# Kernel optimization log

Hardware: AMD Instinct MI355X
Metric: run time of the kernel (lower is better)

The kernel has to match this reference:

```python
import jax, jax.numpy as jnp
import numpy as np

EPS = 1e-5  # torch BatchNorm default

def _conv(x, w, pad):
    return jax.lax.conv_general_dilated(x, w, window_strides=(1, 1), padding=pad,
                                        dimension_numbers=('NCHW', 'OIHW', 'NCHW'))

def _bn(x, g, b, m, v):
    # eval-mode BatchNorm2d over channel axis 1 of NCHW
    scale = g / jnp.sqrt(v + EPS)
    return x * scale[None, :, None, None] + (b - m * scale)[None, :, None, None]

def _bn1d(x, g, b, m, v):
    scale = g / jnp.sqrt(v + EPS)
    return x * scale[None, :] + (b - m * scale)[None, :]

def _prelu(x, a):
    # torch PReLU with num_parameters=1 (scalar slope, init 0.25)
    return jnp.where(x >= 0, x, a * x)

def setup_inputs():
    key = jax.random.key(0)
    ks = jax.random.split(key, 10)
    B, H, W = 256, 600, 19
    C1, C2 = 40, 40
    x = jax.random.normal(ks[0], (B, H, W), jnp.float32)
    w1 = jax.random.normal(ks[1], (C1, 1, 29, 1), jnp.float32) * 0.1
    w2 = jax.random.normal(ks[2], (C2, C1, 1, 19), jnp.float32) * 0.1
    fc1_w = jax.random.uniform(ks[3], (80, 1560), jnp.float32, -0.005, 0.005)
    fc2_w = jax.random.uniform(ks[4], (2, 80), jnp.float32, -0.005, 0.005)
    def bn_params(k, n):
        k1, k2 = jax.random.split(k)
        return (jnp.ones((n,), jnp.float32), jnp.zeros((n,), jnp.float32),
                jax.random.normal(k1, (n,), jnp.float32) * 0.1,
                jax.random.uniform(k2, (n,), jnp.float32, 0.5, 1.5))
    bn1_g, bn1_b, bn1_m, bn1_v = bn_params(ks[5], C1)
    bn2_g, bn2_b, bn2_m, bn2_v = bn_params(ks[6], C2)
    bn3_g, bn3_b, bn3_m, bn3_v = bn_params(ks[7], 80)
    a1 = jnp.full((1,), 0.25, jnp.float32)
    a2 = jnp.full((1,), 0.25, jnp.float32)
    a3 = jnp.full((1,), 0.25, jnp.float32)
    return dict(x=x, w1=w1, bn1_g=bn1_g, bn1_b=bn1_b, bn1_m=bn1_m, bn1_v=bn1_v, a1=a1,
                w2=w2, bn2_g=bn2_g, bn2_b=bn2_b, bn2_m=bn2_m, bn2_v=bn2_v, a2=a2,
                fc1_w=fc1_w, bn3_g=bn3_g, bn3_b=bn3_b, bn3_m=bn3_m, bn3_v=bn3_v, a3=a3,
                fc2_w=fc2_w)

def reference(x, w1, bn1_g, bn1_b, bn1_m, bn1_v, a1,
              w2, bn2_g, bn2_b, bn2_m, bn2_v, a2,
              fc1_w, bn3_g, bn3_b, bn3_m, bn3_v, a3, fc2_w):
    h = x[:, None, :, :]                                  # [B,1,600,19]
    # conv1: inputs NOT binarized, weights sign-binarized
    h = _conv(h, jnp.sign(w1), [(14, 14), (0, 0)])         # [B,40,600,19]
    h = _prelu(_bn(h, bn1_g, bn1_b, bn1_m, bn1_v), a1)
    # conv2: inputs and weights binarized
    h = _conv(jnp.sign(h), jnp.sign(w2), [(0, 0), (0, 0)])  # [B,40,600,1]
    h = _prelu(_bn(h, bn2_g, bn2_b, bn2_m, bn2_v), a2)
    # AvgPool2d kernel (30,1) stride (15,1)
    h = jax.lax.reduce_window(h, 0.0, jax.lax.add, (1, 1, 30, 1), (1, 1, 15, 1), 'VALID') / 30.0  # [B,40,39,1]
    h = h.reshape(h.shape[0], -1)                          # [B,1560]
    # fc1: binarized input/weight; BatchNorm1d; PReLU; dropout is identity in eval
    h = jnp.sign(h) @ jnp.sign(fc1_w).T                    # [B,80]
    h = _prelu(_bn1d(h, bn3_g, bn3_b, bn3_m, bn3_v), a3)
    out = jnp.sign(h) @ jnp.sign(fc2_w).T                  # [B,2]
    return out
```

## Files before the change

kernel.cpp:

```cpp
#include <hip/hip_runtime.h>
#include <stdint.h>

#define B_ 256
#define H_ 600
#define W_ 19
#define C1_ 40
#define C2_ 40
#define KH_ 29
#define PAD_ 14
#define NW_ 760
#define NWORDS_ 12
#define NJ_ 39
#define FIN_ 1560
#define FOUT_ 80
#define FCW_ 25
#define HS1 150
#define XSTL 179

__device__ __forceinline__ float fsgn(float x){ return (x > 0.f) ? 1.f : ((x < 0.f) ? -1.f : 0.f); }
__device__ __forceinline__ int8_t isgn(float x){ return (int8_t)((x > 0.f) - (x < 0.f)); }

__global__ void k0_setup(const float* __restrict__ w1, const float* __restrict__ w2,
                         const float* __restrict__ fc1w, const float* __restrict__ fc2w,
                         const float* __restrict__ g1, const float* __restrict__ b1,
                         const float* __restrict__ m1, const float* __restrict__ v1,
                         const float* __restrict__ g2, const float* __restrict__ b2,
                         const float* __restrict__ m2, const float* __restrict__ v2,
                         const float* __restrict__ g3, const float* __restrict__ b3,
                         const float* __restrict__ m3, const float* __restrict__ v3,
                         float* __restrict__ w1s, uint64_t* __restrict__ w2m,
                         uint64_t* __restrict__ fc1p, int8_t* __restrict__ fc2s,
                         float* __restrict__ bnp)
{
  int tid = blockIdx.x * blockDim.x + threadIdx.x;
  int np  = gridDim.x * blockDim.x;
  int lane = threadIdx.x & 63;
  int gw   = tid >> 6;
  int nw   = np >> 6;

  for (int i = tid; i < C1_*KH_; i += np) w1s[i] = fsgn(w1[i]);

  for (int v = gw; v < C2_*NWORDS_; v += nw){
    int c2 = v / NWORDS_, wd = v % NWORDS_;
    int idx = wd*64 + lane;
    float val = 0.f;
    if (idx < NW_){
      int c1 = idx % 40, w = idx / 40;
      val = w2[c2*NW_ + c1*W_ + w];
    }
    unsigned long long m = __ballot(val > 0.f);
    if (lane == 0) w2m[c2*NWORDS_ + wd] = m;
  }
  for (int v = gw; v < FOUT_*2*FCW_; v += nw){
    int o = v / (2*FCW_), r = v % (2*FCW_);
    int neg = r / FCW_, wd = r % FCW_;
    int e = wd*64 + lane;
    float val = (e < FIN_) ? fc1w[o*FIN_ + e] : 0.f;
    unsigned long long m = __ballot(neg ? (val < 0.f) : (val > 0.f));
    if (lane == 0) fc1p[o*(2*FCW_) + r] = m;
  }
  for (int i = tid; i < 2*FOUT_; i += np) fc2s[i] = isgn(fc2w[i]);
  for (int i = tid; i < C1_; i += np){
    float s = __fdiv_rn(g1[i], __fsqrt_rn(__fadd_rn(v1[i], 1e-5f)));
    bnp[i] = s; bnp[40+i] = __fsub_rn(b1[i], __fmul_rn(m1[i], s));
  }
  for (int i = tid; i < C2_; i += np){
    float s = __fdiv_rn(g2[i], __fsqrt_rn(__fadd_rn(v2[i], 1e-5f)));
    bnp[80+i] = s; bnp[120+i] = __fsub_rn(b2[i], __fmul_rn(m2[i], s));
  }
  for (int i = tid; i < FOUT_; i += np){
    float s = __fdiv_rn(g3[i], __fsqrt_rn(__fadd_rn(v3[i], 1e-5f)));
    bnp[160+i] = s; bnp[240+i] = __fsub_rn(b3[i], __fmul_rn(m3[i], s));
  }
}

__device__ __forceinline__ float opaque(float v){ asm volatile("" : "+v"(v)); return v; }

template<int T>
__device__ __forceinline__ float acc29(float (&xw)[29], float (&wt)[29]){
  float a = 0.f;
  #pragma unroll
  for (int k = 0; k < 29; ++k)
    a = __builtin_fmaf(wt[k], xw[(T + k) % 29], a);
  return a;
}

template<int T>
__device__ __forceinline__ void step1(float (&xw)[29], float (&wt)[29],
                                      const float* xck, ulonglong2* ob,
                                      float scale, float bias, int lane){
  xw[(T + 28) % 29] = opaque(xck[T + 28]);
  float acc = acc29<T>(xw, wt);
  float z = __fadd_rn(__fmul_rn(acc, scale), bias);
  unsigned long long pp = __ballot(z > 0.f);
  unsigned long long nn = __ballot(z < 0.f);
  if (lane == 0){ ulonglong2 v; v.x = pp; v.y = pp | nn; ob[T] = v; }
}

#define S1(t) step1<t>(xw, wt, xck, ob, scale, bias, lane);

__global__ __launch_bounds__(256, 6) void k1_conv1(const float* __restrict__ x,
                                                   const float* __restrict__ w1s,
                                                   const float* __restrict__ bnp,
                                                   uint64_t* __restrict__ s1bits)
{
  __shared__ float xs[W_ * XSTL];
  int b = blockIdx.x, ht = blockIdx.y, g = blockIdx.z;
  int h0 = HS1 * ht;
  const float* xb = x + (size_t)b * H_ * W_;
  for (int i = threadIdx.x; i < (HS1 + 28) * W_; i += 256){
    int r = i / W_, w = i % W_;
    int gh = h0 - PAD_ + r;
    xs[w*XSTL + r] = (gh >= 0 && gh < H_) ? xb[gh*W_ + w] : 0.f;
  }
  __syncthreads();

  int lane = threadIdx.x & 63, wave = threadIdx.x >> 6;
  int wd   = g*4 + wave;
  int idx  = wd*64 + lane;
  bool valid = (idx < NW_);
  int c1 = idx % 40;
  int w  = valid ? (idx / 40) : 18;

  float wt[KH_];
  #pragma unroll
  for (int k = 0; k < KH_; ++k) wt[k] = opaque(w1s[c1*KH_ + k]);
  float scale = bnp[c1], bias = bnp[40 + c1];
  if (!valid){ scale = __builtin_nanf(""); bias = scale; }
  const float* xcol = &xs[w * XSTL];

  float xw[29];
  #pragma unroll
  for (int s = 0; s < 28; ++s) xw[s] = opaque(xcol[s]);

  ulonglong2* obase = (ulonglong2*)s1bits + ((size_t)(b*12 + wd) * H_ + h0);

  #pragma unroll 1
  for (int c = 0; c < 5; ++c){
    const float* xck = xcol + 29*c;
    ulonglong2* ob = obase + 29*c;
    S1(0)  S1(1)  S1(2)  S1(3)  S1(4)  S1(5)  S1(6)  S1(7)  S1(8)  S1(9)
    S1(10) S1(11) S1(12) S1(13) S1(14) S1(15) S1(16) S1(17) S1(18) S1(19)
    S1(20) S1(21) S1(22) S1(23) S1(24) S1(25) S1(26) S1(27) S1(28)
  }
  {
    const float* xck = xcol + 145;
    ulonglong2* ob = obase + 145;
    S1(0) S1(1) S1(2) S1(3) S1(4)
  }
}

__global__ __launch_bounds__(640) void k2_fused(const uint64_t* __restrict__ s1bits,
                                                const uint64_t* __restrict__ w2m_g,
                                                const uint64_t* __restrict__ fc1p,
                                                const int8_t* __restrict__ fc2s,
                                                const float* __restrict__ bnp,
                                                const float* __restrict__ a2p,
                                                const float* __restrict__ a3p,
                                                float* __restrict__ out)
{
  __shared__ float z[C2_][640];
  __shared__ uint64_t spP[FCW_], spN[FCW_];
  __shared__ int z3[FOUT_];
  int b = blockIdx.x;
  int tid = threadIdx.x;
  int lane = tid & 63;
  int rowc = (tid < H_) ? tid : (H_ - 1);

  uint64_t Pv[NWORDS_], Mv[NWORDS_];
  const ulonglong2* sb = (const ulonglong2*)s1bits + (size_t)b * NWORDS_ * H_;
  #pragma unroll
  for (int wd = 0; wd < NWORDS_; ++wd){
    ulonglong2 pm = sb[(size_t)wd * H_ + rowc];
    Pv[wd] = pm.x; Mv[wd] = pm.y;
  }
  int nzv = 0;
  #pragma unroll
  for (int wd = 0; wd < NWORDS_; ++wd) nzv += __popcll(Mv[wd]);

  float alpha2 = a2p[0];
  #pragma unroll 2
  for (int c2 = 0; c2 < C2_; ++c2){
    int dsum = 0;
    #pragma unroll
    for (int wd = 0; wd < NWORDS_; ++wd)
      dsum += __popcll(Mv[wd] & (Pv[wd] ^ w2m_g[c2*NWORDS_ + wd]));
    int y = nzv - 2*dsum;
    float u = __fadd_rn(__fmul_rn((float)y, bnp[80 + c2]), bnp[120 + c2]);
    z[c2][tid] = (u >= 0.f) ? u : __fmul_rn(alpha2, u);
  }
  __syncthreads();

  #pragma unroll 1
  for (int ch = 0; ch < 3; ++ch){
    int o = ch*640 + tid;
    bool act = (o < FIN_);
    int c2 = act ? (o / NJ_) : 0, j = act ? (o % NJ_) : 0;
    int base = 15*j;
    float s = 0.f;
    #pragma unroll
    for (int r = 0; r < 30; ++r) s = __fadd_rn(s, z[c2][base + r]);
    unsigned long long pp = __ballot(act && (s > 0.f));
    unsigned long long nn = __ballot(act && (s < 0.f));
    int word = ch*10 + (tid >> 6);
    if (lane == 0 && word < FCW_){ spP[word] = pp; spN[word] = nn; }
  }
  __syncthreads();

  float alpha3 = a3p[0];
  if (tid < FOUT_){
    int o = tid;
    const uint64_t* wp = fc1p + o * (2*FCW_);
    int acc = 0;
    #pragma unroll
    for (int wd = 0; wd < FCW_; ++wd){
      uint64_t P = spP[wd], N = spN[wd];
      uint64_t WP = wp[wd], WN = wp[FCW_ + wd];
      acc += __popcll(P & WP) + __popcll(N & WN) - __popcll(P & WN) - __popcll(N & WP);
    }
    float u = __fadd_rn(__fmul_rn((float)acc, bnp[160 + o]), bnp[240 + o]);
    float zz = (u >= 0.f) ? u : __fmul_rn(alpha3, u);
    z3[o] = (zz > 0.f) - (zz < 0.f);
  }
  __syncthreads();
  if (tid < 2){
    int acc = 0;
    for (int o = 0; o < FOUT_; ++o) acc += z3[o] * (int)fc2s[tid * FOUT_ + o];
    out[b*2 + tid] = (float)acc;
  }
}

extern "C" void kernel_launch(void* const* d_in, const int* in_sizes, int n_in,
                              void* d_out, int out_size, void* d_ws, size_t ws_size,
                              hipStream_t stream)
{
  const float* x    = (const float*)d_in[0];
  const float* w1   = (const float*)d_in[1];
  const float* g1   = (const float*)d_in[2];
  const float* b1   = (const float*)d_in[3];
  const float* m1   = (const float*)d_in[4];
  const float* v1   = (const float*)d_in[5];
  const float* a1   = (const float*)d_in[6];   (void)a1;
  const float* w2   = (const float*)d_in[7];
  const float* g2   = (const float*)d_in[8];
  const float* b2   = (const float*)d_in[9];
  const float* m2   = (const float*)d_in[10];
  const float* v2   = (const float*)d_in[11];
  const float* a2   = (const float*)d_in[12];
  const float* fc1w = (const float*)d_in[13];
  const float* g3   = (const float*)d_in[14];
  const float* b3   = (const float*)d_in[15];
  const float* m3   = (const float*)d_in[16];
  const float* v3   = (const float*)d_in[17];
  const float* a3   = (const float*)d_in[18];
  const float* fc2w = (const float*)d_in[19];

  char* ws = (char*)d_ws;
  uint64_t* s1bits = (uint64_t*)(ws);
  uint64_t* w2m    = (uint64_t*)(ws + 29491200);
  float*    w1s    = (float*)   (ws + 29495040);
  float*    bnp    = (float*)   (ws + 29499680);
  uint64_t* fc1p   = (uint64_t*)(ws + 29500960);
  int8_t*   fc2s   = (int8_t*)  (ws + 29532960);

  k0_setup<<<dim3(128), dim3(256), 0, stream>>>(w1, w2, fc1w, fc2w,
                                                g1, b1, m1, v1,
                                                g2, b2, m2, v2,
                                                g3, b3, m3, v3,
                                                w1s, w2m, fc1p, fc2s, bnp);
  k1_conv1<<<dim3(B_, 4, 3), dim3(256), 0, stream>>>(x, w1s, bnp, s1bits);
  k2_fused<<<dim3(B_), dim3(640), 0, stream>>>(s1bits, w2m, fc1p, fc2s, bnp,
                                               a2, a3, (float*)d_out);
}
```

Measured before the change: 220.9 us.

## Split fused conv2/pool/fc kernel into per-half-channel conv2pool and separate FC kernel

The single per-batch conv2+pool+fc kernel becomes two kernels. The first runs two blocks per batch, each covering 20 output channels, which halves shared memory per block and doubles the grid. It writes the int8 pooled signs to the workspace, and a small second kernel does fc1/fc2. Separately, conv1 moves to amdgpu_waves_per_eu(6,6), the asm volatile barrier becomes non-volatile, and the setup grid is doubled. This costs an extra launch and a small global round trip.

```diff
diff --git a/kernel.cpp b/kernel.cpp
--- a/kernel.cpp
+++ b/kernel.cpp
@@ -74,7 +74,7 @@
   }
 }
 
-__device__ __forceinline__ float opaque(float v){ asm volatile("" : "+v"(v)); return v; }
+__device__ __forceinline__ float opaque(float v){ asm("" : "+v"(v)); return v; }
 
 template<int T>
 __device__ __forceinline__ float acc29(float (&xw)[29], float (&wt)[29]){
@@ -99,10 +99,12 @@
 
 #define S1(t) step1<t>(xw, wt, xck, ob, scale, bias, lane);
 
-__global__ __launch_bounds__(256, 6) void k1_conv1(const float* __restrict__ x,
-                                                   const float* __restrict__ w1s,
-                                                   const float* __restrict__ bnp,
-                                                   uint64_t* __restrict__ s1bits)
+__global__ __launch_bounds__(256)
+__attribute__((amdgpu_waves_per_eu(6, 6)))
+void k1_conv1(const float* __restrict__ x,
+              const float* __restrict__ w1s,
+              const float* __restrict__ bnp,
+              uint64_t* __restrict__ s1bits)
 {
   __shared__ float xs[W_ * XSTL];
   int b = blockIdx.x, ht = blockIdx.y, g = blockIdx.z;
@@ -150,21 +152,16 @@
   }
 }
 
-__global__ __launch_bounds__(640) void k2_fused(const uint64_t* __restrict__ s1bits,
-                                                const uint64_t* __restrict__ w2m_g,
-                                                const uint64_t* __restrict__ fc1p,
-                                                const int8_t* __restrict__ fc2s,
-                                                const float* __restrict__ bnp,
-                                                const float* __restrict__ a2p,
-                                                const float* __restrict__ a3p,
-                                                float* __restrict__ out)
-{
-  __shared__ float z[C2_][640];
-  __shared__ uint64_t spP[FCW_], spN[FCW_];
-  __shared__ int z3[FOUT_];
-  int b = blockIdx.x;
+__global__ __launch_bounds__(640) void k2a_conv2pool(const uint64_t* __restrict__ s1bits,
+                                                     const uint64_t* __restrict__ w2m_g,
+                                                     const float* __restrict__ bnp,
+                                                     const float* __restrict__ a2p,
+                                                     int8_t* __restrict__ sp)
+{
+  __shared__ float z[20][601];
+  int half = blockIdx.x, b = blockIdx.y;
+  int c2lo = half * 20;
   int tid = threadIdx.x;
-  int lane = tid & 63;
   int rowc = (tid < H_) ? tid : (H_ - 1);
 
   uint64_t Pv[NWORDS_], Mv[NWORDS_];
@@ -180,36 +177,51 @@
 
   float alpha2 = a2p[0];
   #pragma unroll 2
-  for (int c2 = 0; c2 < C2_; ++c2){
+  for (int cl = 0; cl < 20; ++cl){
+    int c2 = c2lo + cl;
     int dsum = 0;
     #pragma unroll
     for (int wd = 0; wd < NWORDS_; ++wd)
       dsum += __popcll(Mv[wd] & (Pv[wd] ^ w2m_g[c2*NWORDS_ + wd]));
     int y = nzv - 2*dsum;
-    float u = __fadd_rn(__fmul_rn((float)y, bnp[80 + c2]), bnp[120 + c2]);
-    z[c2][tid] = (u >= 0.f) ? u : __fmul_rn(alpha2, u);
-  }
-  __syncthreads();
-
-  #pragma unroll 1
-  for (int ch = 0; ch < 3; ++ch){
-    int o = ch*640 + tid;
-    bool act = (o < FIN_);
-    int c2 = act ? (o / NJ_) : 0, j = act ? (o % NJ_) : 0;
+    float u = __fadd_rn(__fmul_rn((float)y, bnp[c2]), bnp[40 + c2]);
+    if (tid < H_) z[cl][tid] = (u >= 0.f) ? u : __fmul_rn(alpha2, u);
+  }
+  __syncthreads();
+
+  for (int o = tid; o < 20*NJ_; o += 640){
+    int cl = o / NJ_, j = o % NJ_;
     int base = 15*j;
     float s = 0.f;
     #pragma unroll
-    for (int r = 0; r < 30; ++r) s = __fadd_rn(s, z[c2][base + r]);
-    unsigned long long pp = __ballot(act && (s > 0.f));
-    unsigned long long nn = __ballot(act && (s < 0.f));
-    int word = ch*10 + (tid >> 6);
-    if (lane == 0 && word < FCW_){ spP[word] = pp; spN[word] = nn; }
-  }
-  __syncthreads();
-
-  float alpha3 = a3p[0];
-  if (tid < FOUT_){
-    int o = tid;
+    for (int r = 0; r < 30; ++r) s = __fadd_rn(s, z[cl][base + r]);
+    sp[(size_t)b*FIN_ + (c2lo + cl)*NJ_ + j] = (int8_t)((s > 0.f) - (s < 0.f));
+  }
+}
+
+__global__ __launch_bounds__(128) void k2b_fc(const int8_t* __restrict__ sp,
+                                              const uint64_t* __restrict__ fc1p,
+                                              const int8_t* __restrict__ fc2s,
+                                              const float* __restrict__ bnp,
+                                              const float* __restrict__ a3p,
+                                              float* __restrict__ out)
+{
+  __shared__ uint64_t spP[FCW_], spN[FCW_];
+  __shared__ int z3[FOUT_];
+  int b = blockIdx.x;
+  int lane = threadIdx.x & 63, wave = threadIdx.x >> 6;
+  const int8_t* spb = sp + (size_t)b * FIN_;
+  for (int wd = wave; wd < FCW_; wd += 2){
+    int e = wd*64 + lane;
+    int v = (e < FIN_) ? (int)spb[e] : 0;
+    unsigned long long p = __ballot(v > 0);
+    unsigned long long n = __ballot(v < 0);
+    if (lane == 0){ spP[wd] = p; spN[wd] = n; }
+  }
+  __syncthreads();
+  float alpha = a3p[0];
+  if (threadIdx.x < FOUT_){
+    int o = threadIdx.x;
     const uint64_t* wp = fc1p + o * (2*FCW_);
     int acc = 0;
     #pragma unroll
@@ -218,15 +230,16 @@
       uint64_t WP = wp[wd], WN = wp[FCW_ + wd];
       acc += __popcll(P & WP) + __popcll(N & WN) - __popcll(P & WN) - __popcll(N & WP);
     }
-    float u = __fadd_rn(__fmul_rn((float)acc, bnp[160 + o]), bnp[240 + o]);
-    float zz = (u >= 0.f) ? u : __fmul_rn(alpha3, u);
-    z3[o] = (zz > 0.f) - (zz < 0.f);
-  }
-  __syncthreads();
-  if (tid < 2){
+    float u = __fadd_rn(__fmul_rn((float)acc, bnp[o]), bnp[80 + o]);
+    float z = (u >= 0.f) ? u : __fmul_rn(alpha, u);
+    z3[o] = (z > 0.f) - (z < 0.f);
+  }
+  __syncthreads();
+  if (threadIdx.x < 2){
+    int k = threadIdx.x;
     int acc = 0;
-    for (int o = 0; o < FOUT_; ++o) acc += z3[o] * (int)fc2s[tid * FOUT_ + o];
-    out[b*2 + tid] = (float)acc;
+    for (int o = 0; o < FOUT_; ++o) acc += z3[o] * (int)fc2s[k * FOUT_ + o];
+    out[b*2 + k] = (float)acc;
   }
 }
 
@@ -262,13 +275,14 @@
   float*    bnp    = (float*)   (ws + 29499680);
   uint64_t* fc1p   = (uint64_t*)(ws + 29500960);
   int8_t*   fc2s   = (int8_t*)  (ws + 29532960);
-
-  k0_setup<<<dim3(128), dim3(256), 0, stream>>>(w1, w2, fc1w, fc2w,
+  int8_t*   sp     = (int8_t*)  (ws + 29533120);
+
+  k0_setup<<<dim3(256), dim3(256), 0, stream>>>(w1, w2, fc1w, fc2w,
                                                 g1, b1, m1, v1,
                                                 g2, b2, m2, v2,
                                                 g3, b3, m3, v3,
                                                 w1s, w2m, fc1p, fc2s, bnp);
   k1_conv1<<<dim3(B_, 4, 3), dim3(256), 0, stream>>>(x, w1s, bnp, s1bits);
-  k2_fused<<<dim3(B_), dim3(640), 0, stream>>>(s1bits, w2m, fc1p, fc2s, bnp,
-                                               a2, a3, (float*)d_out);
-}
+  k2a_conv2pool<<<dim3(2, B_), dim3(640), 0, stream>>>(s1bits, w2m, bnp + 80, a2, sp);
+  k2b_fc<<<dim3(B_), dim3(128), 0, stream>>>(sp, fc1p, fc2s, bnp + 160, a3, (float*)d_out);
+}
```

Result: no change. 221.7 us (+0.4%).
